# Performance work log

Measured on AMD Instinct MI355X. Metric: run time of the kernel, lower is better.

The kernel has to match this reference:

```python
import jax, jax.numpy as jnp
import numpy as np
import math

B, S, D = 2, 2048, 1024
H, DK, DV = 16, 64, 64
DFF = 4096
EPS = 1e-6


def _layer_norm(x, g, b):
    mu = jnp.mean(x, axis=-1, keepdims=True)
    var = jnp.var(x, axis=-1, keepdims=True)
    return (x - mu) * jax.lax.rsqrt(var + EPS) * g + b


def setup_inputs() -> dict:
    key = jax.random.key(0)
    ks = jax.random.split(key, 8)
    s_attn = 0.02
    return {
        "enc_input": jax.random.normal(ks[0], (B, S, D), dtype=jnp.float32),
        # attention projections (torch Linear weight layout [out, in])
        "w_qs": jax.random.normal(ks[1], (H * DK, D), dtype=jnp.float32) * s_attn,
        "w_ks": jax.random.normal(ks[2], (H * DK, D), dtype=jnp.float32) * s_attn,
        "w_vs": jax.random.normal(ks[3], (H * DV, D), dtype=jnp.float32) * s_attn,
        "fc_w": jax.random.normal(ks[4], (D, H * DV), dtype=jnp.float32) * s_attn,
        "fc_b": jnp.zeros((D,), dtype=jnp.float32),
        "ln1_g": jnp.ones((D,), dtype=jnp.float32),
        "ln1_b": jnp.zeros((D,), dtype=jnp.float32),
        # feed-forward
        "ffn_w1": jax.random.normal(ks[5], (DFF, D), dtype=jnp.float32) * s_attn,
        "ffn_b1": jnp.zeros((DFF,), dtype=jnp.float32),
        "ffn_w2": jax.random.normal(ks[6], (D, DFF), dtype=jnp.float32) * s_attn,
        "ffn_b2": jnp.zeros((D,), dtype=jnp.float32),
        "ln2_g": jnp.ones((D,), dtype=jnp.float32),
        "ln2_b": jnp.zeros((D,), dtype=jnp.float32),
    }


def reference(enc_input, w_qs, w_ks, w_vs, fc_w, fc_b, ln1_g, ln1_b,
              ffn_w1, ffn_b1, ffn_w2, ffn_b2, ln2_g, ln2_b):
    # --- MultiHeadAttention (normalize_before=True, dropout=eval/identity) ---
    residual = enc_input
    q_in = _layer_norm(enc_input, ln1_g, ln1_b)
    # NB: torch code only pre-normalizes q; k/v use the raw input
    q = (q_in @ w_qs.T).reshape(B, S, H, DK).transpose(0, 2, 1, 3)   # [B,H,S,DK]
    k = (enc_input @ w_ks.T).reshape(B, S, H, DK).transpose(0, 2, 1, 3)
    v = (enc_input @ w_vs.T).reshape(B, S, H, DV).transpose(0, 2, 1, 3)
    scale = 1.0 / math.sqrt(DK)
    scores = jnp.einsum("bhqd,bhkd->bhqk", q * scale, k)             # [B,H,S,S]
    attn = jax.nn.softmax(scores, axis=-1)
    ctx = jnp.einsum("bhqk,bhkd->bhqd", attn, v)                     # [B,H,S,DV]
    ctx = ctx.transpose(0, 2, 1, 3).reshape(B, S, H * DV)
    attn_out = ctx @ fc_w.T + fc_b + residual

    # --- PositionwiseFeedForward (pre-norm, exact GELU) ---
    res2 = attn_out
    h = _layer_norm(attn_out, ln2_g, ln2_b)
    h = jax.nn.gelu(h @ ffn_w1.T + ffn_b1, approximate=False)
    enc_output = h @ ffn_w2.T + ffn_b2 + res2
    return enc_output, attn
```

## Files before the change

### kernel.cpp

```cpp
#include <hip/hip_runtime.h>
#include <hip/hip_bf16.h>
#include <math.h>

typedef __attribute__((ext_vector_type(8))) short bf16x8;
typedef __attribute__((ext_vector_type(4))) float f32x4;
typedef __attribute__((ext_vector_type(4))) unsigned short u16x4;

namespace {
constexpr int kB = 2, kS = 2048, kD = 1024, kH = 16, kDK = 64, kDV = 64, kDFF = 4096;
constexpr float kEps = 1e-6f;
constexpr int kM = kB * kS;
}

__device__ inline float fast_exp2(float x) {
    return __builtin_amdgcn_exp2f(x);
}

__device__ inline unsigned short f2bf(float f) {
    unsigned int u = __builtin_bit_cast(unsigned int, f);
    u += 0x7fffu + ((u >> 16) & 1u);
    return (unsigned short)(u >> 16);
}
__device__ inline float bf2f(unsigned short u) {
    unsigned int x = ((unsigned int)u) << 16;
    return __builtin_bit_cast(float, x);
}

__device__ inline void gload_lds16(const void* g, void* l) {
    __builtin_amdgcn_global_load_lds(
        (const __attribute__((address_space(1))) unsigned int*)g,
        (__attribute__((address_space(3))) unsigned int*)l, 16, 0, 0);
}

__global__ __launch_bounds__(256) void cvt_weights(
    const float* __restrict__ s_wqs, const float* __restrict__ s_wks,
    const float* __restrict__ s_wvs, const float* __restrict__ s_fcw,
    const float* __restrict__ s_w1,  const float* __restrict__ s_w2,
    unsigned short* __restrict__ dst)
{
    const int total = 3145728;
    int i = blockIdx.x * 256 + threadIdx.x;
    const int stride = gridDim.x * 256;
    for (; i < total; i += stride) {
        const float* src; int off;
        if      (i <  262144) { src = s_wqs; off = i; }
        else if (i <  524288) { src = s_wks; off = i -  262144; }
        else if (i <  786432) { src = s_wvs; off = i -  524288; }
        else if (i < 1048576) { src = s_fcw; off = i -  786432; }
        else if (i < 2097152) { src = s_w1;  off = i - 1048576; }
        else                  { src = s_w2;  off = i - 2097152; }
        const float4 v = ((const float4*)src)[off];
        u16x4 o;
        o.x = f2bf(v.x); o.y = f2bf(v.y); o.z = f2bf(v.z); o.w = f2bf(v.w);
        ((u16x4*)dst)[i] = o;
    }
}

template<bool DUAL>
__global__ __launch_bounds__(256) void ln_bf16_kernel(
    const float* __restrict__ x, const float* __restrict__ g,
    const float* __restrict__ b, unsigned short* __restrict__ out,
    unsigned short* __restrict__ out_raw)
{
    const size_t row = blockIdx.x;
    const float4 v = ((const float4*)(x + row * kD))[threadIdx.x];
    if (DUAL) {
        u16x4 r;
        r.x = f2bf(v.x); r.y = f2bf(v.y); r.z = f2bf(v.z); r.w = f2bf(v.w);
        ((u16x4*)(out_raw + row * kD))[threadIdx.x] = r;
    }
    float s = v.x + v.y + v.z + v.w;
    float q = v.x * v.x + v.y * v.y + v.z * v.z + v.w * v.w;
#pragma unroll
    for (int off = 32; off > 0; off >>= 1) {
        s += __shfl_down(s, off);
        q += __shfl_down(q, off);
    }
    __shared__ float rs[4], rq[4];
    const int wid = threadIdx.x >> 6, lane = threadIdx.x & 63;
    if (lane == 0) { rs[wid] = s; rq[wid] = q; }
    __syncthreads();
    const float ts = rs[0] + rs[1] + rs[2] + rs[3];
    const float tq = rq[0] + rq[1] + rq[2] + rq[3];
    const float mean = ts * (1.0f / kD);
    const float var  = tq * (1.0f / kD) - mean * mean;
    const float rstd = rsqrtf(var + kEps);
    const float4 gg = ((const float4*)g)[threadIdx.x];
    const float4 bb = ((const float4*)b)[threadIdx.x];
    u16x4 o;
    o.x = f2bf((v.x - mean) * rstd * gg.x + bb.x);
    o.y = f2bf((v.y - mean) * rstd * gg.y + bb.y);
    o.z = f2bf((v.z - mean) * rstd * gg.z + bb.z);
    o.w = f2bf((v.w - mean) * rstd * gg.w + bb.w);
    ((u16x4*)(out + row * kD))[threadIdx.x] = o;
}

__global__ __launch_bounds__(256) void qkv_gemm(
    const unsigned short* __restrict__ qinb,
    const unsigned short* __restrict__ xb,
    const unsigned short* __restrict__ wq,
    const unsigned short* __restrict__ wk,
    const unsigned short* __restrict__ wv,
    unsigned short* __restrict__ Qb,
    unsigned short* __restrict__ Kb,
    unsigned short* __restrict__ Vt)
{
    __shared__ __align__(16) unsigned short As[128 * 32];
    __shared__ __align__(16) unsigned short Bs[128 * 32];

    const int m0  = blockIdx.y * 128;
    const int n0g = blockIdx.x * 128;
    const int which = n0g >> 10;
    const int n0  = n0g & 1023;
    const unsigned short* A = (which == 0) ? qinb : xb;
    const unsigned short* B = (which == 0) ? wq : (which == 1 ? wk : wv);

    const int t = threadIdx.x;
    const int w = t >> 6, lane = t & 63;
    const int wm = (w >> 1) * 64;
    const int wn = (w & 1) * 64;

    f32x4 acc[4][4];
#pragma unroll
    for (int m = 0; m < 4; ++m)
#pragma unroll
        for (int n = 0; n < 4; ++n) acc[m][n] = (f32x4){0.f, 0.f, 0.f, 0.f};

    for (int k0 = 0; k0 < kD; k0 += 32) {
#pragma unroll
        for (int i = 0; i < 2; ++i) {
            const int r = i * 64 + (t >> 2);
            gload_lds16(A + (size_t)(m0 + r) * kD + k0 + (t & 3) * 8,
                        As + r * 32 + (t & 3) * 8);
            gload_lds16(B + (size_t)(n0 + r) * kD + k0 + (t & 3) * 8,
                        Bs + r * 32 + (t & 3) * 8);
        }
        __syncthreads();

        bf16x8 a[4], bb[4];
#pragma unroll
        for (int m = 0; m < 4; ++m)
            a[m] = *(const bf16x8*)(As + (wm + m * 16 + (lane & 15)) * 32 + (lane >> 4) * 8);
#pragma unroll
        for (int n = 0; n < 4; ++n)
            bb[n] = *(const bf16x8*)(Bs + (wn + n * 16 + (lane & 15)) * 32 + (lane >> 4) * 8);
#pragma unroll
        for (int m = 0; m < 4; ++m)
#pragma unroll
            for (int n = 0; n < 4; ++n)
                acc[m][n] = __builtin_amdgcn_mfma_f32_16x16x32_bf16(a[m], bb[n], acc[m][n], 0, 0, 0);
        __syncthreads();
    }

    const int col = lane & 15, rb = (lane >> 4) * 4;
#pragma unroll
    for (int m = 0; m < 4; ++m)
#pragma unroll
        for (int n = 0; n < 4; ++n)
#pragma unroll
            for (int j = 0; j < 4; ++j) {
                const int gm  = m0 + wm + m * 16 + rb + j;
                const int gnl = n0 + wn + n * 16 + col;
                const unsigned short bv = f2bf(acc[m][n][j]);
                if (which == 0)
                    Qb[(size_t)gm * kD + gnl] = bv;
                else if (which == 1)
                    Kb[(size_t)gm * kD + gnl] = bv;
                else
                    Vt[((size_t)(gm >> 11) * kD + gnl) * kS + (gm & 2047)] = bv;
            }
}

template<int BN, bool OUTB, bool BIAS, bool RES, bool GELU>
__global__ __launch_bounds__(256) void gemm_mfma(
    const unsigned short* __restrict__ A, int lda,
    const unsigned short* __restrict__ B, int ldb,
    void* __restrict__ Cbase, int ldc,
    const float* __restrict__ bias,
    const float* __restrict__ resbase, int ldres,
    int K)
{
    __shared__ __align__(16) unsigned short As[128 * 32];
    __shared__ __align__(16) unsigned short Bs[BN * 32];

    float* Cf = (float*)Cbase;
    unsigned short* Cu = (unsigned short*)Cbase;

    const int m0 = blockIdx.y * 128;
    const int n0 = blockIdx.x * BN;
    const int t = threadIdx.x;
    const int w = t >> 6, lane = t & 63;
    const int wm = (w >> 1) * 64;
    const int wn = (w & 1) * (BN / 2);
    constexpr int AN = (BN / 2) / 16;

    f32x4 acc[4][AN];
#pragma unroll
    for (int m = 0; m < 4; ++m)
#pragma unroll
        for (int n = 0; n < AN; ++n) acc[m][n] = (f32x4){0.f, 0.f, 0.f, 0.f};

    for (int k0 = 0; k0 < K; k0 += 32) {
#pragma unroll
        for (int i = 0; i < 2; ++i) {
            const int r = i * 64 + (t >> 2);
            gload_lds16(A + (size_t)(m0 + r) * lda + k0 + (t & 3) * 8,
                        As + r * 32 + (t & 3) * 8);
        }
#pragma unroll
        for (int i = 0; i < BN / 64; ++i) {
            const int r = i * 64 + (t >> 2);
            gload_lds16(B + (size_t)(n0 + r) * ldb + k0 + (t & 3) * 8,
                        Bs + r * 32 + (t & 3) * 8);
        }
        __syncthreads();

        bf16x8 a[4], bb[AN];
#pragma unroll
        for (int m = 0; m < 4; ++m)
            a[m] = *(const bf16x8*)(As + (wm + m * 16 + (lane & 15)) * 32 + (lane >> 4) * 8);
#pragma unroll
        for (int n = 0; n < AN; ++n)
            bb[n] = *(const bf16x8*)(Bs + (wn + n * 16 + (lane & 15)) * 32 + (lane >> 4) * 8);
#pragma unroll
        for (int m = 0; m < 4; ++m)
#pragma unroll
            for (int n = 0; n < AN; ++n)
                acc[m][n] = __builtin_amdgcn_mfma_f32_16x16x32_bf16(a[m], bb[n], acc[m][n], 0, 0, 0);
        __syncthreads();
    }

    const int col = lane & 15, rb = (lane >> 4) * 4;
#pragma unroll
    for (int m = 0; m < 4; ++m)
#pragma unroll
        for (int n = 0; n < AN; ++n)
#pragma unroll
            for (int j = 0; j < 4; ++j) {
                const int gm = m0 + wm + m * 16 + rb + j;
                const int gn = n0 + wn + n * 16 + col;
                float v = acc[m][n][j];
                if (BIAS) v += bias[gn];
                if (GELU) v = 0.5f * v * (1.0f + erff(v * 0.7071067811865476f));
                if (RES)  v += resbase[(size_t)gm * ldres + gn];
                if (OUTB) Cu[(size_t)gm * ldc + gn] = f2bf(v);
                else      Cf[(size_t)gm * ldc + gn] = v;
            }
}

__global__ __launch_bounds__(256) void gemm_splitk(
    const unsigned short* __restrict__ A, int lda,
    const unsigned short* __restrict__ B, int ldb,
    float* __restrict__ P,
    int ldc, int K, int split)
{
    __shared__ __align__(16) unsigned short As[128 * 32];
    __shared__ __align__(16) unsigned short Bs[128 * 32];

    const int m0 = blockIdx.y * 128;
    const int n0 = blockIdx.x * 128;
    const int kz = blockIdx.z;
    const int Kc = K / split;
    const int kbase = kz * Kc;
    float* Pz = P + (size_t)kz * kM * ldc;

    const int t = threadIdx.x;
    const int w = t >> 6, lane = t & 63;
    const int wm = (w >> 1) * 64;
    const int wn = (w & 1) * 64;

    f32x4 acc[4][4];
#pragma unroll
    for (int m = 0; m < 4; ++m)
#pragma unroll
        for (int n = 0; n < 4; ++n) acc[m][n] = (f32x4){0.f, 0.f, 0.f, 0.f};

    for (int k0 = kbase; k0 < kbase + Kc; k0 += 32) {
#pragma unroll
        for (int i = 0; i < 2; ++i) {
            const int r = i * 64 + (t >> 2);
            gload_lds16(A + (size_t)(m0 + r) * lda + k0 + (t & 3) * 8,
                        As + r * 32 + (t & 3) * 8);
            gload_lds16(B + (size_t)(n0 + r) * ldb + k0 + (t & 3) * 8,
                        Bs + r * 32 + (t & 3) * 8);
        }
        __syncthreads();

        bf16x8 a[4], bb[4];
#pragma unroll
        for (int m = 0; m < 4; ++m)
            a[m] = *(const bf16x8*)(As + (wm + m * 16 + (lane & 15)) * 32 + (lane >> 4) * 8);
#pragma unroll
        for (int n = 0; n < 4; ++n)
            bb[n] = *(const bf16x8*)(Bs + (wn + n * 16 + (lane & 15)) * 32 + (lane >> 4) * 8);
#pragma unroll
        for (int m = 0; m < 4; ++m)
#pragma unroll
            for (int n = 0; n < 4; ++n)
                acc[m][n] = __builtin_amdgcn_mfma_f32_16x16x32_bf16(a[m], bb[n], acc[m][n], 0, 0, 0);
        __syncthreads();
    }

    const int col = lane & 15, rb = (lane >> 4) * 4;
#pragma unroll
    for (int m = 0; m < 4; ++m)
#pragma unroll
        for (int n = 0; n < 4; ++n)
#pragma unroll
            for (int j = 0; j < 4; ++j) {
                const int gm = m0 + wm + m * 16 + rb + j;
                const int gn = n0 + wn + n * 16 + col;
                Pz[(size_t)gm * ldc + gn] = acc[m][n][j];
            }
}

__global__ __launch_bounds__(256) void reduce_out(
    const float* __restrict__ p0, const float* __restrict__ p1,
    const float* __restrict__ bias, const float* __restrict__ res,
    float* __restrict__ out, int n4)
{
    int i = blockIdx.x * 256 + threadIdx.x;
    const int stride = gridDim.x * 256;
    for (; i < n4; i += stride) {
        const float4 a = ((const float4*)p0)[i];
        const float4 b = ((const float4*)p1)[i];
        const float4 bi = ((const float4*)bias)[i & 255];
        const float4 r = ((const float4*)res)[i];
        float4 o;
        o.x = a.x + b.x + bi.x + r.x;
        o.y = a.y + b.y + bi.y + r.y;
        o.z = a.z + b.z + bi.z + r.z;
        o.w = a.w + b.w + bi.w + r.w;
        ((float4*)out)[i] = o;
    }
}

__global__ __launch_bounds__(256) void fused_attn(
    const unsigned short* __restrict__ Qb,
    const unsigned short* __restrict__ Kb,
    const unsigned short* __restrict__ Vt,
    float* __restrict__ attn,
    unsigned short* __restrict__ ctx)
{
    __shared__ __align__(16) unsigned short KVs[128][72];
    __shared__ __align__(16) unsigned short Ps[64][72];

    const int z = blockIdx.y, b = z >> 4, h = z & 15;
    const int qt = blockIdx.x;
    const int t = threadIdx.x, w = t >> 6, lane = t & 63;
    const int l16 = lane & 15, lhi = lane >> 4;

    const unsigned short* Qp = Qb + (size_t)b * kS * kD + (size_t)h * kDK;
    const unsigned short* Kp = Kb + (size_t)b * kS * kD + (size_t)h * kDK;
    const unsigned short* Vp = Vt + (size_t)(b * kD + h * kDV) * kS;
    float* Ap = attn + (size_t)z * kS * kS;

    bf16x8 q[2];
    const int qrow0 = qt * 64 + w * 16;
#pragma unroll
    for (int kq = 0; kq < 2; ++kq) {
        bf16x8 v = *(const bf16x8*)(Qp + (size_t)(qrow0 + l16) * kD + kq * 32 + lhi * 8);
#pragma unroll
        for (int e = 0; e < 8; ++e)
            v[e] = (short)f2bf(bf2f((unsigned short)v[e]) * 0.18033688011112042f);
        q[kq] = v;
    }

    float lrow[4] = {0.f, 0.f, 0.f, 0.f};

    for (int kt = 0; kt < 16; ++kt) {
#pragma unroll
        for (int i = 0; i < 4; ++i) {
            const int r = i * 32 + (t >> 3), c = (t & 7) * 8;
            *(bf16x8*)&KVs[r][c] = *(const bf16x8*)(Kp + (size_t)(kt * 128 + r) * kD + c);
        }
        __syncthreads();

        f32x4 s[8];
#pragma unroll
        for (int n = 0; n < 8; ++n) s[n] = (f32x4){0.f, 0.f, 0.f, 0.f};
#pragma unroll
        for (int kq = 0; kq < 2; ++kq)
#pragma unroll
            for (int n = 0; n < 8; ++n) {
                const bf16x8 kf = *(const bf16x8*)&KVs[n * 16 + l16][kq * 32 + lhi * 8];
                s[n] = __builtin_amdgcn_mfma_f32_16x16x32_bf16(q[kq], kf, s[n], 0, 0, 0);
            }

#pragma unroll
        for (int j = 0; j < 4; ++j) {
            float sum = ((fast_exp2(s[0][j]) + fast_exp2(s[1][j]))
                       + (fast_exp2(s[2][j]) + fast_exp2(s[3][j])))
                      + ((fast_exp2(s[4][j]) + fast_exp2(s[5][j]))
                       + (fast_exp2(s[6][j]) + fast_exp2(s[7][j])));
#pragma unroll
            for (int off = 1; off < 16; off <<= 1) sum += __shfl_xor(sum, off);
            lrow[j] += sum;
        }
        __syncthreads();
    }

    float invl[4];
#pragma unroll
    for (int j = 0; j < 4; ++j) invl[j] = 1.0f / lrow[j];

    f32x4 o[4];
#pragma unroll
    for (int n = 0; n < 4; ++n) o[n] = (f32x4){0.f, 0.f, 0.f, 0.f};

    for (int kt = 0; kt < 32; ++kt) {
#pragma unroll
        for (int i = 0; i < 2; ++i) {
            const int r = i * 32 + (t >> 3), c = (t & 7) * 8;
            *(bf16x8*)&KVs[r][c]      = *(const bf16x8*)(Kp + (size_t)(kt * 64 + r) * kD + c);
            *(bf16x8*)&KVs[64 + r][c] = *(const bf16x8*)(Vp + (size_t)r * kS + kt * 64 + c);
        }
        __syncthreads();

        f32x4 s[4];
#pragma unroll
        for (int n = 0; n < 4; ++n) s[n] = (f32x4){0.f, 0.f, 0.f, 0.f};
#pragma unroll
        for (int kq = 0; kq < 2; ++kq)
#pragma unroll
            for (int n = 0; n < 4; ++n) {
                const bf16x8 kf = *(const bf16x8*)&KVs[n * 16 + l16][kq * 32 + lhi * 8];
                s[n] = __builtin_amdgcn_mfma_f32_16x16x32_bf16(q[kq], kf, s[n], 0, 0, 0);
            }

#pragma unroll
        for (int j = 0; j < 4; ++j) {
            const int qrow_l = w * 16 + lhi * 4 + j;
#pragma unroll
            for (int n = 0; n < 4; ++n) {
                const float p = fast_exp2(s[n][j]) * invl[j];
                Ps[qrow_l][n * 16 + l16] = f2bf(p);
            }
        }
        __syncthreads();

#pragma unroll
        for (int rg = 0; rg < 2; ++rg) {
            const int row = rg * 32 + (t >> 3);
            const int cb  = (t & 7) * 8;
            const bf16x8 pv = *(const bf16x8*)&Ps[row][cb];
            f32x4 f0, f1;
            f0.x = bf2f((unsigned short)pv[0]); f0.y = bf2f((unsigned short)pv[1]);
            f0.z = bf2f((unsigned short)pv[2]); f0.w = bf2f((unsigned short)pv[3]);
            f1.x = bf2f((unsigned short)pv[4]); f1.y = bf2f((unsigned short)pv[5]);
            f1.z = bf2f((unsigned short)pv[6]); f1.w = bf2f((unsigned short)pv[7]);
            float* dst = Ap + (size_t)(qt * 64 + row) * kS + kt * 64 + cb;
            __builtin_nontemporal_store(f0, (f32x4*)dst);
            __builtin_nontemporal_store(f1, (f32x4*)(dst + 4));
        }

#pragma unroll
        for (int ks = 0; ks < 2; ++ks) {
            const bf16x8 pa = *(const bf16x8*)&Ps[w * 16 + l16][ks * 32 + lhi * 8];
#pragma unroll
            for (int n = 0; n < 4; ++n) {
                const bf16x8 vf = *(const bf16x8*)&KVs[64 + n * 16 + l16][ks * 32 + lhi * 8];
                o[n] = __builtin_amdgcn_mfma_f32_16x16x32_bf16(pa, vf, o[n], 0, 0, 0);
            }
        }
        __syncthreads();
    }

#pragma unroll
    for (int n = 0; n < 4; ++n)
#pragma unroll
        for (int j = 0; j < 4; ++j) {
            const int qg = qt * 64 + w * 16 + lhi * 4 + j;
            const int dv = n * 16 + l16;
            ctx[((size_t)b * kS + qg) * kD + h * kDV + dv] = f2bf(o[n][j]);
        }
}

extern "C" void kernel_launch(void* const* d_in, const int* in_sizes, int n_in,
                              void* d_out, int out_size, void* d_ws, size_t ws_size,
                              hipStream_t stream) {
    (void)in_sizes; (void)n_in; (void)out_size; (void)ws_size;

    const float* x      = (const float*)d_in[0];
    const float* w_qs   = (const float*)d_in[1];
    const float* w_ks   = (const float*)d_in[2];
    const float* w_vs   = (const float*)d_in[3];
    const float* fc_w   = (const float*)d_in[4];
    const float* fc_b   = (const float*)d_in[5];
    const float* ln1_g  = (const float*)d_in[6];
    const float* ln1_b  = (const float*)d_in[7];
    const float* ffn_w1 = (const float*)d_in[8];
    const float* ffn_b1 = (const float*)d_in[9];
    const float* ffn_w2 = (const float*)d_in[10];
    const float* ffn_b2 = (const float*)d_in[11];
    const float* ln2_g  = (const float*)d_in[12];
    const float* ln2_b  = (const float*)d_in[13];

    float* out_enc  = (float*)d_out;
    float* out_attn = out_enc + (size_t)kM * kD;

    unsigned short* xb   = (unsigned short*)d_ws;
    unsigned short* qinb = xb   + (size_t)4194304;
    unsigned short* Qb   = qinb + (size_t)4194304;
    unsigned short* Kb   = Qb   + (size_t)4194304;
    unsigned short* Vt   = Kb   + (size_t)4194304;
    unsigned short* ctxb = Vt   + (size_t)4194304;
    unsigned short* hb   = ctxb + (size_t)4194304;
    unsigned short* gb   = hb   + (size_t)4194304;
    unsigned short* wqsb = gb   + (size_t)16777216;
    unsigned short* wksb = wqsb + (size_t)1048576;
    unsigned short* wvsb = wksb + (size_t)1048576;
    unsigned short* fcwb = wvsb + (size_t)1048576;
    unsigned short* w1b  = fcwb + (size_t)1048576;
    unsigned short* w2b  = w1b  + (size_t)4194304;
    float* attn_out      = (float*)(w2b + (size_t)4194304);

    float* part0 = (float*)xb;
    float* part1 = (float*)Qb;

    const dim3 blk(256);

    cvt_weights<<<2048, blk, 0, stream>>>(w_qs, w_ks, w_vs, fc_w, ffn_w1, ffn_w2, wqsb);

    ln_bf16_kernel<true><<<kM, blk, 0, stream>>>(x, ln1_g, ln1_b, qinb, xb);

    qkv_gemm<<<dim3(24, 32), blk, 0, stream>>>(qinb, xb, wqsb, wksb, wvsb, Qb, Kb, Vt);

    fused_attn<<<dim3(32, 32), blk, 0, stream>>>(Qb, Kb, Vt, out_attn, ctxb);

    gemm_mfma<64, false, true, true, false><<<dim3(16, 32), blk, 0, stream>>>(
        ctxb, kD, fcwb, kD, attn_out, kD, fc_b, x, kD, kD);

    ln_bf16_kernel<false><<<kM, blk, 0, stream>>>(attn_out, ln2_g, ln2_b, hb, nullptr);

    gemm_mfma<128, true, true, false, true><<<dim3(32, 32), blk, 0, stream>>>(
        hb, kD, w1b, kD, gb, kDFF, ffn_b1, nullptr, 0, kD);

    gemm_splitk<<<dim3(8, 32, 2), blk, 0, stream>>>(
        gb, kDFF, w2b, kDFF, part0, kD, kDFF, 2);
    reduce_out<<<2048, blk, 0, stream>>>(part0, part1, ffn_b2, attn_out,
                                         out_enc, kM * kD / 4);
}
```

Baseline: 441.7 us.

## Replace split-K FFN2 GEMM and reduction with single 64x128-tile GEMM with fused epilogue

Adds a BM template parameter to gemm_mfma so it can use 64x128 output tiles. The second FFN GEMM now runs as one kernel over 512 blocks with bias and residual fused into its epilogue, replacing the two-way split-K kernel and its separate reduce pass. This removes the fp32 partial-sum round trip and one launch, but each block now walks the full K=4096. The fc projection also switches from 128x64 to 64x128 tiles.

Measured after the change: 446.8 us. Within noise of the previous version (+1.2%).

```diff
diff --git a/kernel.cpp b/kernel.cpp
--- a/kernel.cpp
+++ b/kernel.cpp
@@ -171,7 +171,7 @@
             }
 }
 
-template<int BN, bool OUTB, bool BIAS, bool RES, bool GELU>
+template<int BM, int BN, bool OUTB, bool BIAS, bool RES, bool GELU>
 __global__ __launch_bounds__(256) void gemm_mfma(
     const unsigned short* __restrict__ A, int lda,
     const unsigned short* __restrict__ B, int ldb,
@@ -180,29 +180,30 @@
     const float* __restrict__ resbase, int ldres,
     int K)
 {
-    __shared__ __align__(16) unsigned short As[128 * 32];
+    __shared__ __align__(16) unsigned short As[BM * 32];
     __shared__ __align__(16) unsigned short Bs[BN * 32];
 
     float* Cf = (float*)Cbase;
     unsigned short* Cu = (unsigned short*)Cbase;
 
-    const int m0 = blockIdx.y * 128;
+    const int m0 = blockIdx.y * BM;
     const int n0 = blockIdx.x * BN;
     const int t = threadIdx.x;
     const int w = t >> 6, lane = t & 63;
-    const int wm = (w >> 1) * 64;
+    const int wm = (w >> 1) * (BM / 2);
     const int wn = (w & 1) * (BN / 2);
+    constexpr int AM = (BM / 2) / 16;
     constexpr int AN = (BN / 2) / 16;
 
-    f32x4 acc[4][AN];
-#pragma unroll
-    for (int m = 0; m < 4; ++m)
+    f32x4 acc[AM][AN];
+#pragma unroll
+    for (int m = 0; m < AM; ++m)
 #pragma unroll
         for (int n = 0; n < AN; ++n) acc[m][n] = (f32x4){0.f, 0.f, 0.f, 0.f};
 
     for (int k0 = 0; k0 < K; k0 += 32) {
 #pragma unroll
-        for (int i = 0; i < 2; ++i) {
+        for (int i = 0; i < BM / 64; ++i) {
             const int r = i * 64 + (t >> 2);
             gload_lds16(A + (size_t)(m0 + r) * lda + k0 + (t & 3) * 8,
                         As + r * 32 + (t & 3) * 8);
@@ -215,15 +216,15 @@
         }
         __syncthreads();
 
-        bf16x8 a[4], bb[AN];
-#pragma unroll
-        for (int m = 0; m < 4; ++m)
+        bf16x8 a[AM], bb[AN];
+#pragma unroll
+        for (int m = 0; m < AM; ++m)
             a[m] = *(const bf16x8*)(As + (wm + m * 16 + (lane & 15)) * 32 + (lane >> 4) * 8);
 #pragma unroll
         for (int n = 0; n < AN; ++n)
             bb[n] = *(const bf16x8*)(Bs + (wn + n * 16 + (lane & 15)) * 32 + (lane >> 4) * 8);
 #pragma unroll
-        for (int m = 0; m < 4; ++m)
+        for (int m = 0; m < AM; ++m)
 #pragma unroll
             for (int n = 0; n < AN; ++n)
                 acc[m][n] = __builtin_amdgcn_mfma_f32_16x16x32_bf16(a[m], bb[n], acc[m][n], 0, 0, 0);
@@ -232,7 +233,7 @@
 
     const int col = lane & 15, rb = (lane >> 4) * 4;
 #pragma unroll
-    for (int m = 0; m < 4; ++m)
+    for (int m = 0; m < AM; ++m)
 #pragma unroll
         for (int n = 0; n < AN; ++n)
 #pragma unroll
@@ -246,93 +247,6 @@
                 if (OUTB) Cu[(size_t)gm * ldc + gn] = f2bf(v);
                 else      Cf[(size_t)gm * ldc + gn] = v;
             }
-}
-
-__global__ __launch_bounds__(256) void gemm_splitk(
-    const unsigned short* __restrict__ A, int lda,
-    const unsigned short* __restrict__ B, int ldb,
-    float* __restrict__ P,
-    int ldc, int K, int split)
-{
-    __shared__ __align__(16) unsigned short As[128 * 32];
-    __shared__ __align__(16) unsigned short Bs[128 * 32];
-
-    const int m0 = blockIdx.y * 128;
-    const int n0 = blockIdx.x * 128;
-    const int kz = blockIdx.z;
-    const int Kc = K / split;
-    const int kbase = kz * Kc;
-    float* Pz = P + (size_t)kz * kM * ldc;
-
-    const int t = threadIdx.x;
-    const int w = t >> 6, lane = t & 63;
-    const int wm = (w >> 1) * 64;
-    const int wn = (w & 1) * 64;
-
-    f32x4 acc[4][4];
-#pragma unroll
-    for (int m = 0; m < 4; ++m)
-#pragma unroll
-        for (int n = 0; n < 4; ++n) acc[m][n] = (f32x4){0.f, 0.f, 0.f, 0.f};
-
-    for (int k0 = kbase; k0 < kbase + Kc; k0 += 32) {
-#pragma unroll
-        for (int i = 0; i < 2; ++i) {
-            const int r = i * 64 + (t >> 2);
-            gload_lds16(A + (size_t)(m0 + r) * lda + k0 + (t & 3) * 8,
-                        As + r * 32 + (t & 3) * 8);
-            gload_lds16(B + (size_t)(n0 + r) * ldb + k0 + (t & 3) * 8,
-                        Bs + r * 32 + (t & 3) * 8);
-        }
-        __syncthreads();
-
-        bf16x8 a[4], bb[4];
-#pragma unroll
-        for (int m = 0; m < 4; ++m)
-            a[m] = *(const bf16x8*)(As + (wm + m * 16 + (lane & 15)) * 32 + (lane >> 4) * 8);
-#pragma unroll
-        for (int n = 0; n < 4; ++n)
-            bb[n] = *(const bf16x8*)(Bs + (wn + n * 16 + (lane & 15)) * 32 + (lane >> 4) * 8);
-#pragma unroll
-        for (int m = 0; m < 4; ++m)
-#pragma unroll
-            for (int n = 0; n < 4; ++n)
-                acc[m][n] = __builtin_amdgcn_mfma_f32_16x16x32_bf16(a[m], bb[n], acc[m][n], 0, 0, 0);
-        __syncthreads();
-    }
-
-    const int col = lane & 15, rb = (lane >> 4) * 4;
-#pragma unroll
-    for (int m = 0; m < 4; ++m)
-#pragma unroll
-        for (int n = 0; n < 4; ++n)
-#pragma unroll
-            for (int j = 0; j < 4; ++j) {
-                const int gm = m0 + wm + m * 16 + rb + j;
-                const int gn = n0 + wn + n * 16 + col;
-                Pz[(size_t)gm * ldc + gn] = acc[m][n][j];
-            }
-}
-
-__global__ __launch_bounds__(256) void reduce_out(
-    const float* __restrict__ p0, const float* __restrict__ p1,
-    const float* __restrict__ bias, const float* __restrict__ res,
-    float* __restrict__ out, int n4)
-{
-    int i = blockIdx.x * 256 + threadIdx.x;
-    const int stride = gridDim.x * 256;
-    for (; i < n4; i += stride) {
-        const float4 a = ((const float4*)p0)[i];
-        const float4 b = ((const float4*)p1)[i];
-        const float4 bi = ((const float4*)bias)[i & 255];
-        const float4 r = ((const float4*)res)[i];
-        float4 o;
-        o.x = a.x + b.x + bi.x + r.x;
-        o.y = a.y + b.y + bi.y + r.y;
-        o.z = a.z + b.z + bi.z + r.z;
-        o.w = a.w + b.w + bi.w + r.w;
-        ((float4*)out)[i] = o;
-    }
 }
 
 __global__ __launch_bounds__(256) void fused_attn(
@@ -515,9 +429,6 @@
     unsigned short* w2b  = w1b  + (size_t)4194304;
     float* attn_out      = (float*)(w2b + (size_t)4194304);
 
-    float* part0 = (float*)xb;
-    float* part1 = (float*)Qb;
-
     const dim3 blk(256);
 
     cvt_weights<<<2048, blk, 0, stream>>>(w_qs, w_ks, w_vs, fc_w, ffn_w1, ffn_w2, wqsb);
@@ -528,16 +439,14 @@
 
     fused_attn<<<dim3(32, 32), blk, 0, stream>>>(Qb, Kb, Vt, out_attn, ctxb);
 
-    gemm_mfma<64, false, true, true, false><<<dim3(16, 32), blk, 0, stream>>>(
+    gemm_mfma<64, 128, false, true, true, false><<<dim3(8, 64), blk, 0, stream>>>(
         ctxb, kD, fcwb, kD, attn_out, kD, fc_b, x, kD, kD);
 
     ln_bf16_kernel<false><<<kM, blk, 0, stream>>>(attn_out, ln2_g, ln2_b, hb, nullptr);
 
-    gemm_mfma<128, true, true, false, true><<<dim3(32, 32), blk, 0, stream>>>(
+    gemm_mfma<128, 128, true, true, false, true><<<dim3(32, 32), blk, 0, stream>>>(
         hb, kD, w1b, kD, gb, kDFF, ffn_b1, nullptr, 0, kD);
 
-    gemm_splitk<<<dim3(8, 32, 2), blk, 0, stream>>>(
-        gb, kDFF, w2b, kDFF, part0, kD, kDFF, 2);
-    reduce_out<<<2048, blk, 0, stream>>>(part0, part1, ffn_b2, attn_out,
-                                         out_enc, kM * kD / 4);
-}
+    gemm_mfma<64, 128, false, true, true, false><<<dim3(8, 64), blk, 0, stream>>>(
+        gb, kDFF, w2b, kDFF, out_enc, kD, ffn_b2, attn_out, kD, kDFF);
+}
```
